# Performance work log

Measured on AMD Instinct MI355X. Metric: run time of the kernel, lower is better.

Reference implementation:

```python
import jax, jax.numpy as jnp
import numpy as np

D_MODEL = 768
N_HEAD = 12
D_FF = 3072
EPS = 1e-5


def _layer_norm(x, w, b):
    mu = jnp.mean(x, axis=-1, keepdims=True)
    var = jnp.mean(jnp.square(x - mu), axis=-1, keepdims=True)
    return (x - mu) * jax.lax.rsqrt(var + EPS) * w + b


def setup_inputs() -> dict:
    key = jax.random.key(0)
    ks = jax.random.split(key, 8)
    B, S, D = 2, 4096, D_MODEL
    s_in = 1.0 / np.sqrt(D)
    s_ff = 1.0 / np.sqrt(D_FF)
    return {
        "src": jax.random.normal(ks[0], (B, S, D), jnp.float32),
        "w_qkv": jax.random.uniform(ks[1], (3 * D, D), jnp.float32, -s_in, s_in),
        "b_qkv": jnp.zeros((3 * D,), jnp.float32),
        "w_out": jax.random.uniform(ks[2], (D, D), jnp.float32, -s_in, s_in),
        "b_out": jnp.zeros((D,), jnp.float32),
        "w1": jax.random.uniform(ks[3], (D_FF, D), jnp.float32, -s_in, s_in),
        "b1": jnp.zeros((D_FF,), jnp.float32),
        "w2": jax.random.uniform(ks[4], (D, D_FF), jnp.float32, -s_ff, s_ff),
        "b2": jnp.zeros((D,), jnp.float32),
        "ln1_w": jnp.ones((D,), jnp.float32),
        "ln1_b": jnp.zeros((D,), jnp.float32),
        "ln2_w": jnp.ones((D,), jnp.float32),
        "ln2_b": jnp.zeros((D,), jnp.float32),
    }


def reference(src, w_qkv, b_qkv, w_out, b_out, w1, b1, w2, b2,
              ln1_w, ln1_b, ln2_w, ln2_b):
    B, S, D = src.shape
    H, dh = N_HEAD, D // N_HEAD
    # fused QKV projection: [B,S,3D]
    qkv = jnp.einsum('bsd,ed->bse', src, w_qkv) + b_qkv
    q, k, v = jnp.split(qkv, 3, axis=-1)
    q = q.reshape(B, S, H, dh)
    k = k.reshape(B, S, H, dh)
    v = v.reshape(B, S, H, dh)
    scale = 1.0 / np.sqrt(dh)
    scores = jnp.einsum('bqhd,bkhd->bhqk', q, k) * scale  # [B,H,S,S]
    attn = jax.nn.softmax(scores, axis=-1)
    ctx = jnp.einsum('bhqk,bkhd->bqhd', attn, v).reshape(B, S, D)
    attn_out = jnp.einsum('bsd,ed->bse', ctx, w_out) + b_out
    # post-norm residual (norm_first=False), dropout inactive in eval
    x = _layer_norm(src + attn_out, ln1_w, ln1_b)
    h = jax.nn.relu(jnp.einsum('bsd,fd->bsf', x, w1) + b1)
    ffn = jnp.einsum('bsf,df->bsd', h, w2) + b2
    return _layer_norm(x + ffn, ln2_w, ln2_b)
```

## Files before the change

### kernel.cpp

```cpp
#include <hip/hip_runtime.h>
#include <hip/hip_bf16.h>

typedef __hip_bfloat16 bf16;
typedef __attribute__((ext_vector_type(8))) short s16x8;
typedef __attribute__((ext_vector_type(4))) float f32x4;

#define MFMA16x16x32(A, B, C) __builtin_amdgcn_mfma_f32_16x16x32_bf16((A), (B), (C), 0, 0, 0)

__device__ __forceinline__ void async_copy16(const bf16* g, bf16* l) {
  __builtin_amdgcn_global_load_lds(
      (const __attribute__((address_space(1))) void*)g,
      (__attribute__((address_space(3))) void*)l, 16, 0, 0);
}

__device__ __forceinline__ int SW(int row, int chunk) {
  return row * 64 + (((chunk) ^ (row & 7)) << 3);
}

__global__ __launch_bounds__(256)
void cast_f2b_kernel(const float* __restrict__ in, bf16* __restrict__ out, int n) {
  const int i = (blockIdx.x * 256 + threadIdx.x) * 4;
  if (i < n) {
    const float4 f = *(const float4*)(in + i);
    out[i + 0] = (bf16)f.x; out[i + 1] = (bf16)f.y;
    out[i + 2] = (bf16)f.z; out[i + 3] = (bf16)f.w;
  }
}

template <int RELU, int VT, int ACCUM, typename OutT>
__global__ __launch_bounds__(256)
void gemm_bt_kernel(const bf16* __restrict__ A, const bf16* __restrict__ B,
                    const float* __restrict__ bias, OutT* __restrict__ C,
                    int N, int K, int ldb) {
  __shared__ __align__(16) bf16 As[128 * 32];
  __shared__ __align__(16) bf16 Bs[128 * 32];

  const int t = threadIdx.x;
  const int lane = t & 63;
  const int wave = t >> 6;
  const int wm = (wave >> 1) << 6;
  const int wn = (wave & 1) << 6;
  const int col16 = lane & 15;
  const int quad = lane >> 4;
  const int bm = blockIdx.x;
  const int bn = blockIdx.y;

  const bf16* Ag = A + (size_t)(bm * 128 + (t >> 2)) * K + (t & 3) * 8;
  const bf16* Bg = B + (size_t)(bn * 128 + (t >> 2)) * ldb + (t & 3) * 8;
  bf16* Asd = As + t * 8;
  bf16* Bsd = Bs + t * 8;

  f32x4 acc[4][4] = {};

  for (int k0 = 0; k0 < K; k0 += 32) {
    __syncthreads();
    async_copy16(Ag + k0, Asd);
    async_copy16(Ag + (size_t)64 * K + k0, Asd + 2048);
    async_copy16(Bg + k0, Bsd);
    async_copy16(Bg + (size_t)64 * ldb + k0, Bsd + 2048);
    asm volatile("s_waitcnt vmcnt(0)" ::: "memory");
    __syncthreads();

    s16x8 af[4], bfr[4];
#pragma unroll
    for (int i = 0; i < 4; i++)
      af[i] = *(const s16x8*)(As + (wm + i * 16 + col16) * 32 + quad * 8);
#pragma unroll
    for (int j = 0; j < 4; j++)
      bfr[j] = *(const s16x8*)(Bs + (wn + j * 16 + col16) * 32 + quad * 8);
#pragma unroll
    for (int i = 0; i < 4; i++)
#pragma unroll
      for (int j = 0; j < 4; j++)
        acc[i][j] = MFMA16x16x32(af[i], bfr[j], acc[i][j]);
  }

  const int row0 = bm * 128 + wm + quad * 4;
  const int col0 = bn * 128 + wn + col16;
#pragma unroll
  for (int j = 0; j < 4; j++) {
    const int col = col0 + j * 16;
    const float bv = ACCUM ? 0.0f : bias[col];
#pragma unroll
    for (int i = 0; i < 4; i++) {
#pragma unroll
      for (int r = 0; r < 4; r++) {
        float v = acc[i][j][r] + bv;
        if (RELU) v = fmaxf(v, 0.0f);
        const int row = row0 + i * 16 + r;
        if (VT) {
          ((bf16*)C)[(size_t)((row >> 12) * 12 + (col >> 6)) * 262144 +
                     (col & 63) * 4096 + (row & 4095)] = (bf16)v;
        } else {
          const size_t idx = (size_t)row * N + col;
          if (ACCUM) v += ((const float*)C)[idx];
          C[idx] = (OutT)v;
        }
      }
    }
  }
}

__global__ __launch_bounds__(256)
void attn_kernel(const bf16* __restrict__ QK, const bf16* __restrict__ Vt,
                 bf16* __restrict__ Opart, float* __restrict__ lbuf) {
  __shared__ __align__(16) bf16 Ks[2][64 * 64];
  __shared__ __align__(16) bf16 Vs[2][64 * 64];
  __shared__ __align__(16) bf16 Ps[4][32 * 64];

  const int t = threadIdx.x, lane = t & 63, wave = t >> 6;
  const int col16 = lane & 15, quad = lane >> 4;
  const int b = blockIdx.z, h = blockIdx.y;
  const int ks = blockIdx.x >> 5;
  const int qblk = blockIdx.x & 31;
  const int qw0 = qblk * 128 + wave * 32;

  s16x8 bq[2][2];
#pragma unroll
  for (int qt = 0; qt < 2; qt++)
#pragma unroll
    for (int s = 0; s < 2; s++) {
      union { s16x8 v; bf16 hh[8]; } u;
      u.v = *(const s16x8*)(QK + (size_t)(b * 4096 + qw0 + qt * 16 + col16) * 1536 +
                            h * 64 + s * 32 + quad * 8);
#pragma unroll
      for (int e = 0; e < 8; e++) u.hh[e] = (bf16)((float)u.hh[e] * 0.18033688f);
      bq[qt][s] = u.v;
    }

  union { s16x8 v; short s_[8]; } uo1;
#pragma unroll
  for (int e = 0; e < 8; e++) uo1.s_[e] = (short)0x3F80;
  const s16x8 aones = uo1.v;

  const int srow = t >> 3;
  const int schx = (t & 7) ^ (srow & 7);
  const bf16* kgb = QK + (size_t)(b * 4096) * 1536 + 768 + h * 64;
  const bf16* vgb = Vt + (size_t)(b * 12 + h) * 262144;
  const bf16* ksrc0 = kgb + (size_t)srow * 1536 + schx * 8;
  const bf16* ksrc1 = kgb + (size_t)(32 + srow) * 1536 + schx * 8;
  const bf16* vsrc0 = vgb + (size_t)srow * 4096 + schx * 8;
  const bf16* vsrc1 = vgb + (size_t)(32 + srow) * 4096 + schx * 8;

  f32x4 o[4][2] = {};
  f32x4 lacc[2] = {};
  bf16* pw = &Ps[wave][0];

  const int kbeg = ks * 2048, kend = kbeg + 2048;

  async_copy16(ksrc0 + (size_t)kbeg * 1536, &Ks[0][0] + t * 8);
  async_copy16(ksrc1 + (size_t)kbeg * 1536, &Ks[0][0] + 2048 + t * 8);
  async_copy16(vsrc0 + kbeg, &Vs[0][0] + t * 8);
  async_copy16(vsrc1 + kbeg, &Vs[0][0] + 2048 + t * 8);

  int n = 0;
  for (int k0 = kbeg; k0 < kend; k0 += 64, n ^= 1) {
    __syncthreads();
    if (k0 + 64 < kend) {
      const int k1 = k0 + 64;
      async_copy16(ksrc0 + (size_t)k1 * 1536, &Ks[n ^ 1][0] + t * 8);
      async_copy16(ksrc1 + (size_t)k1 * 1536, &Ks[n ^ 1][0] + 2048 + t * 8);
      async_copy16(vsrc0 + k1, &Vs[n ^ 1][0] + t * 8);
      async_copy16(vsrc1 + k1, &Vs[n ^ 1][0] + 2048 + t * 8);
    }
    const bf16* ksn = &Ks[n][0];
    const bf16* vsn = &Vs[n][0];

    f32x4 st[4][2] = {};
#pragma unroll
    for (int s = 0; s < 2; s++) {
      s16x8 ak[4];
#pragma unroll
      for (int kt = 0; kt < 4; kt++)
        ak[kt] = *(const s16x8*)(ksn + SW(kt * 16 + col16, s * 4 + quad));
#pragma unroll
      for (int kt = 0; kt < 4; kt++)
#pragma unroll
        for (int qt = 0; qt < 2; qt++)
          st[kt][qt] = MFMA16x16x32(ak[kt], bq[qt][s], st[kt][qt]);
    }

#pragma unroll
    for (int qt = 0; qt < 2; qt++) {
#pragma unroll
      for (int kt = 0; kt < 4; kt++) {
        union { unsigned long long u; bf16 hh[4]; } pk;
#pragma unroll
        for (int r = 0; r < 4; r++)
          pk.hh[r] = (bf16)__builtin_amdgcn_exp2f(st[kt][qt][r]);
        *(unsigned long long*)(pw + (qt * 16 + col16) * 64 +
                               (((kt * 2 + (quad >> 1)) ^ (col16 & 7)) << 3) +
                               (quad & 1) * 4) = pk.u;
      }
    }
    asm volatile("s_waitcnt lgkmcnt(0)" ::: "memory");

#pragma unroll
    for (int s = 0; s < 2; s++) {
      s16x8 bp[2];
#pragma unroll
      for (int qt = 0; qt < 2; qt++)
        bp[qt] = *(const s16x8*)(pw + SW(qt * 16 + col16, s * 4 + quad));
#pragma unroll
      for (int qt = 0; qt < 2; qt++)
        lacc[qt] = MFMA16x16x32(aones, bp[qt], lacc[qt]);
#pragma unroll
      for (int dt = 0; dt < 4; dt++) {
        const s16x8 av = *(const s16x8*)(vsn + SW(dt * 16 + col16, s * 4 + quad));
#pragma unroll
        for (int qt = 0; qt < 2; qt++)
          o[dt][qt] = MFMA16x16x32(av, bp[qt], o[dt][qt]);
      }
    }
  }

  if (lane < 16) {
#pragma unroll
    for (int qt = 0; qt < 2; qt++)
      lbuf[(size_t)ks * 98304 + (size_t)(b * 4096 + qw0 + qt * 16 + lane) * 12 + h] =
          lacc[qt][0];
  }

#pragma unroll
  for (int qt = 0; qt < 2; qt++)
#pragma unroll
    for (int dt = 0; dt < 4; dt++)
#pragma unroll
      for (int r = 0; r < 4; r++)
        pw[(qt * 16 + col16) * 64 + (((dt * 2 + (quad >> 1)) ^ (col16 & 7)) << 3) +
           (quad & 1) * 4 + r] = (bf16)(o[dt][qt][r]);
  asm volatile("s_waitcnt lgkmcnt(0)" ::: "memory");
  const int qrow = lane >> 1, chalf = (lane & 1) * 4;
  bf16* dst = Opart + (size_t)ks * 6291456 +
              (size_t)(b * 4096 + qw0 + qrow) * 768 + h * 64 + chalf * 8;
#pragma unroll
  for (int i = 0; i < 4; i++)
    *(s16x8*)(dst + i * 8) = *(const s16x8*)(pw + SW(qrow, chalf + i));
}

__global__ __launch_bounds__(256)
void attn_combine_kernel(const bf16* __restrict__ Opart,
                         const float* __restrict__ lbuf,
                         bf16* __restrict__ ctx) {
  const int i = blockIdx.x * 256 + threadIdx.x;
  const int row = i / 96, c8 = i % 96;
  const int h = c8 >> 3;
  const float inv = 1.0f / (lbuf[(size_t)row * 12 + h] +
                            lbuf[98304 + (size_t)row * 12 + h]);
  union { s16x8 v; bf16 hh[8]; } ua, ub, uo;
  ua.v = *(const s16x8*)(Opart + (size_t)row * 768 + c8 * 8);
  ub.v = *(const s16x8*)(Opart + 6291456 + (size_t)row * 768 + c8 * 8);
#pragma unroll
  for (int j = 0; j < 8; j++)
    uo.hh[j] = (bf16)(((float)ua.hh[j] + (float)ub.hh[j]) * inv);
  *(s16x8*)(ctx + (size_t)row * 768 + c8 * 8) = uo.v;
}

__global__ __launch_bounds__(256)
void add_ln_b_kernel(const float* __restrict__ X, const float* __restrict__ Y,
                     const float* __restrict__ w, const float* __restrict__ b,
                     bf16* __restrict__ out) {
  const int row = blockIdx.x * 4 + (threadIdx.x >> 6);
  const int lane = threadIdx.x & 63;
  const float* x = X + (size_t)row * 768;
  const float* y = Y + (size_t)row * 768;
  float v[12];
  float s = 0.0f;
#pragma unroll
  for (int i = 0; i < 3; i++) {
    const int c = lane * 4 + i * 256;
    const float4 xf = *(const float4*)(x + c);
    const float4 yf = *(const float4*)(y + c);
    v[i * 4 + 0] = xf.x + yf.x; v[i * 4 + 1] = xf.y + yf.y;
    v[i * 4 + 2] = xf.z + yf.z; v[i * 4 + 3] = xf.w + yf.w;
    s += v[i * 4] + v[i * 4 + 1] + v[i * 4 + 2] + v[i * 4 + 3];
  }
#pragma unroll
  for (int off = 32; off > 0; off >>= 1) s += __shfl_xor(s, off, 64);
  const float mu = s * (1.0f / 768.0f);
  float var = 0.0f;
#pragma unroll
  for (int i = 0; i < 12; i++) { const float d = v[i] - mu; var += d * d; }
#pragma unroll
  for (int off = 32; off > 0; off >>= 1) var += __shfl_xor(var, off, 64);
  const float rs = rsqrtf(var * (1.0f / 768.0f) + 1e-5f);
#pragma unroll
  for (int i = 0; i < 12; i++) {
    const int c = lane * 4 + (i >> 2) * 256 + (i & 3);
    out[(size_t)row * 768 + c] = (bf16)((v[i] - mu) * rs * w[c] + b[c]);
  }
}

__global__ __launch_bounds__(256)
void add_ln_f_kernel(const bf16* __restrict__ X, const float* __restrict__ Y,
                     const float* __restrict__ w, const float* __restrict__ b,
                     float* __restrict__ out) {
  const int row = blockIdx.x * 4 + (threadIdx.x >> 6);
  const int lane = threadIdx.x & 63;
  const bf16* x = X + (size_t)row * 768;
  const float* y = Y + (size_t)row * 768;
  float v[12];
  float s = 0.0f;
#pragma unroll
  for (int i = 0; i < 3; i++) {
    const int c = lane * 4 + i * 256;
    const float4 yf = *(const float4*)(y + c);
    v[i * 4 + 0] = (float)x[c + 0] + yf.x; v[i * 4 + 1] = (float)x[c + 1] + yf.y;
    v[i * 4 + 2] = (float)x[c + 2] + yf.z; v[i * 4 + 3] = (float)x[c + 3] + yf.w;
    s += v[i * 4] + v[i * 4 + 1] + v[i * 4 + 2] + v[i * 4 + 3];
  }
#pragma unroll
  for (int off = 32; off > 0; off >>= 1) s += __shfl_xor(s, off, 64);
  const float mu = s * (1.0f / 768.0f);
  float var = 0.0f;
#pragma unroll
  for (int i = 0; i < 12; i++) { const float d = v[i] - mu; var += d * d; }
#pragma unroll
  for (int off = 32; off > 0; off >>= 1) var += __shfl_xor(var, off, 64);
  const float rs = rsqrtf(var * (1.0f / 768.0f) + 1e-5f);
#pragma unroll
  for (int i = 0; i < 12; i++) {
    const int c = lane * 4 + (i >> 2) * 256 + (i & 3);
    out[(size_t)row * 768 + c] = (v[i] - mu) * rs * w[c] + b[c];
  }
}

extern "C" void kernel_launch(void* const* d_in, const int* in_sizes, int n_in,
                              void* d_out, int out_size, void* d_ws, size_t ws_size,
                              hipStream_t stream) {
  (void)in_sizes; (void)n_in; (void)out_size; (void)ws_size;
  const float* src   = (const float*)d_in[0];
  const float* w_qkv = (const float*)d_in[1];
  const float* b_qkv = (const float*)d_in[2];
  const float* w_out = (const float*)d_in[3];
  const float* b_out = (const float*)d_in[4];
  const float* w1    = (const float*)d_in[5];
  const float* b1    = (const float*)d_in[6];
  const float* w2    = (const float*)d_in[7];
  const float* b2    = (const float*)d_in[8];
  const float* ln1w  = (const float*)d_in[9];
  const float* ln1b  = (const float*)d_in[10];
  const float* ln2w  = (const float*)d_in[11];
  const float* ln2b  = (const float*)d_in[12];
  float* out = (float*)d_out;

  char* ws = (char*)d_ws;
  bf16* wqkvb = (bf16*)ws;
  bf16* woutb = (bf16*)(ws + 3538944);
  bf16* w1b   = (bf16*)(ws + 4718592);
  bf16* w2b   = (bf16*)(ws + 9437184);
  bf16* srcb  = (bf16*)(ws + 14155776);
  bf16* QK    = (bf16*)(ws + 26738688);
  bf16* Vt    = (bf16*)(ws + 51904512);
  bf16* Opart = (bf16*)d_out;
  float* lbuf = (float*)ws;
  bf16* ctx   = (bf16*)(ws + 14155776);
  float* attn_out = (float*)(ws + 26738688);
  bf16* x1b   = (bf16*)(ws + 51904512);
  bf16* hbuf  = (bf16*)(ws + 14155776);
  float* ffn  = out;

  cast_f2b_kernel<<<1728, 256, 0, stream>>>(w_qkv, wqkvb, 2304 * 768);
  cast_f2b_kernel<<<576,  256, 0, stream>>>(w_out, woutb, 768 * 768);
  cast_f2b_kernel<<<2304, 256, 0, stream>>>(w1, w1b, 3072 * 768);
  cast_f2b_kernel<<<2304, 256, 0, stream>>>(w2, w2b, 768 * 3072);
  cast_f2b_kernel<<<6144, 256, 0, stream>>>(src, srcb, 8192 * 768);

  gemm_bt_kernel<0, 0, 0, bf16><<<dim3(64, 12), 256, 0, stream>>>(
      srcb, wqkvb, b_qkv, QK, 1536, 768, 768);
  gemm_bt_kernel<0, 1, 0, bf16><<<dim3(64, 6), 256, 0, stream>>>(
      srcb, wqkvb + (size_t)1536 * 768, b_qkv + 1536, Vt, 768, 768, 768);
  attn_kernel<<<dim3(64, 12, 2), 256, 0, stream>>>(QK, Vt, Opart, lbuf);
  attn_combine_kernel<<<3072, 256, 0, stream>>>(Opart, lbuf, ctx);
  gemm_bt_kernel<0, 0, 0, float><<<dim3(64, 6), 256, 0, stream>>>(
      ctx, woutb, b_out, attn_out, 768, 768, 768);
  add_ln_b_kernel<<<2048, 256, 0, stream>>>(src, attn_out, ln1w, ln1b, x1b);
  for (int c = 0; c < 2; c++) {
    gemm_bt_kernel<1, 0, 0, bf16><<<dim3(64, 12), 256, 0, stream>>>(
        x1b, w1b + (size_t)c * 1536 * 768, b1 + c * 1536, hbuf, 1536, 768, 768);
    if (c == 0)
      gemm_bt_kernel<0, 0, 0, float><<<dim3(64, 6), 256, 0, stream>>>(
          hbuf, w2b + c * 1536, b2, ffn, 768, 1536, 3072);
    else
      gemm_bt_kernel<0, 0, 1, float><<<dim3(64, 6), 256, 0, stream>>>(
          hbuf, w2b + c * 1536, b2, ffn, 768, 1536, 3072);
  }
  add_ln_f_kernel<<<2048, 256, 0, stream>>>(x1b, ffn, ln2w, ln2b, out);
}
```

Before: 494.3 us.

## Double-buffer GEMM LDS tiles and fuse QKV and V-transpose GEMM launches

The GEMM kernel now keeps two LDS buffers for the A and B tiles. It issues the async global-to-LDS copies for the next K step before computing on the current one, so load latency overlaps the MFMA work. The explicit vmcnt wait is dropped, so correctness depends on the barrier waiting for outstanding loads. Separately, the QK and V projections run as a single launch: an epilogue mode writes columns below 1536 row-major and the rest into the transposed V layout. This removes one launch and fills the grid better, at the cost of double the shared memory per block.

```diff
diff --git a/kernel.cpp b/kernel.cpp
--- a/kernel.cpp
+++ b/kernel.cpp
@@ -31,9 +31,9 @@
 __global__ __launch_bounds__(256)
 void gemm_bt_kernel(const bf16* __restrict__ A, const bf16* __restrict__ B,
                     const float* __restrict__ bias, OutT* __restrict__ C,
-                    int N, int K, int ldb) {
-  __shared__ __align__(16) bf16 As[128 * 32];
-  __shared__ __align__(16) bf16 Bs[128 * 32];
+                    int N, int K, int ldb, bf16* __restrict__ C2) {
+  __shared__ __align__(16) bf16 As[2][128 * 32];
+  __shared__ __align__(16) bf16 Bs[2][128 * 32];
 
   const int t = threadIdx.x;
   const int lane = t & 63;
@@ -47,27 +47,34 @@
 
   const bf16* Ag = A + (size_t)(bm * 128 + (t >> 2)) * K + (t & 3) * 8;
   const bf16* Bg = B + (size_t)(bn * 128 + (t >> 2)) * ldb + (t & 3) * 8;
-  bf16* Asd = As + t * 8;
-  bf16* Bsd = Bs + t * 8;
 
   f32x4 acc[4][4] = {};
 
-  for (int k0 = 0; k0 < K; k0 += 32) {
+  async_copy16(Ag, &As[0][0] + t * 8);
+  async_copy16(Ag + (size_t)64 * K, &As[0][0] + 2048 + t * 8);
+  async_copy16(Bg, &Bs[0][0] + t * 8);
+  async_copy16(Bg + (size_t)64 * ldb, &Bs[0][0] + 2048 + t * 8);
+
+  int n = 0;
+  for (int k0 = 0; k0 < K; k0 += 32, n ^= 1) {
     __syncthreads();
-    async_copy16(Ag + k0, Asd);
-    async_copy16(Ag + (size_t)64 * K + k0, Asd + 2048);
-    async_copy16(Bg + k0, Bsd);
-    async_copy16(Bg + (size_t)64 * ldb + k0, Bsd + 2048);
-    asm volatile("s_waitcnt vmcnt(0)" ::: "memory");
-    __syncthreads();
+    if (k0 + 32 < K) {
+      const int k1 = k0 + 32;
+      async_copy16(Ag + k1, &As[n ^ 1][0] + t * 8);
+      async_copy16(Ag + (size_t)64 * K + k1, &As[n ^ 1][0] + 2048 + t * 8);
+      async_copy16(Bg + k1, &Bs[n ^ 1][0] + t * 8);
+      async_copy16(Bg + (size_t)64 * ldb + k1, &Bs[n ^ 1][0] + 2048 + t * 8);
+    }
+    const bf16* asn = &As[n][0];
+    const bf16* bsn = &Bs[n][0];
 
     s16x8 af[4], bfr[4];
 #pragma unroll
     for (int i = 0; i < 4; i++)
-      af[i] = *(const s16x8*)(As + (wm + i * 16 + col16) * 32 + quad * 8);
+      af[i] = *(const s16x8*)(asn + (wm + i * 16 + col16) * 32 + quad * 8);
 #pragma unroll
     for (int j = 0; j < 4; j++)
-      bfr[j] = *(const s16x8*)(Bs + (wn + j * 16 + col16) * 32 + quad * 8);
+      bfr[j] = *(const s16x8*)(bsn + (wn + j * 16 + col16) * 32 + quad * 8);
 #pragma unroll
     for (int i = 0; i < 4; i++)
 #pragma unroll
@@ -88,9 +95,17 @@
         float v = acc[i][j][r] + bv;
         if (RELU) v = fmaxf(v, 0.0f);
         const int row = row0 + i * 16 + r;
-        if (VT) {
+        if (VT == 1) {
           ((bf16*)C)[(size_t)((row >> 12) * 12 + (col >> 6)) * 262144 +
                      (col & 63) * 4096 + (row & 4095)] = (bf16)v;
+        } else if (VT == 2) {
+          if (col < 1536) {
+            C[(size_t)row * N + col] = (OutT)v;
+          } else {
+            const int cc = col - 1536;
+            C2[(size_t)((row >> 12) * 12 + (cc >> 6)) * 262144 +
+               (cc & 63) * 4096 + (row & 4095)] = (bf16)v;
+          }
         } else {
           const size_t idx = (size_t)row * N + col;
           if (ACCUM) v += ((const float*)C)[idx];
@@ -366,24 +381,23 @@
   cast_f2b_kernel<<<2304, 256, 0, stream>>>(w2, w2b, 768 * 3072);
   cast_f2b_kernel<<<6144, 256, 0, stream>>>(src, srcb, 8192 * 768);
 
-  gemm_bt_kernel<0, 0, 0, bf16><<<dim3(64, 12), 256, 0, stream>>>(
-      srcb, wqkvb, b_qkv, QK, 1536, 768, 768);
-  gemm_bt_kernel<0, 1, 0, bf16><<<dim3(64, 6), 256, 0, stream>>>(
-      srcb, wqkvb + (size_t)1536 * 768, b_qkv + 1536, Vt, 768, 768, 768);
+  gemm_bt_kernel<0, 2, 0, bf16><<<dim3(64, 18), 256, 0, stream>>>(
+      srcb, wqkvb, b_qkv, QK, 1536, 768, 768, Vt);
   attn_kernel<<<dim3(64, 12, 2), 256, 0, stream>>>(QK, Vt, Opart, lbuf);
   attn_combine_kernel<<<3072, 256, 0, stream>>>(Opart, lbuf, ctx);
   gemm_bt_kernel<0, 0, 0, float><<<dim3(64, 6), 256, 0, stream>>>(
-      ctx, woutb, b_out, attn_out, 768, 768, 768);
+      ctx, woutb, b_out, attn_out, 768, 768, 768, nullptr);
   add_ln_b_kernel<<<2048, 256, 0, stream>>>(src, attn_out, ln1w, ln1b, x1b);
   for (int c = 0; c < 2; c++) {
     gemm_bt_kernel<1, 0, 0, bf16><<<dim3(64, 12), 256, 0, stream>>>(
-        x1b, w1b + (size_t)c * 1536 * 768, b1 + c * 1536, hbuf, 1536, 768, 768);
+        x1b, w1b + (size_t)c * 1536 * 768, b1 + c * 1536, hbuf, 1536, 768, 768,
+        nullptr);
     if (c == 0)
       gemm_bt_kernel<0, 0, 0, float><<<dim3(64, 6), 256, 0, stream>>>(
-          hbuf, w2b + c * 1536, b2, ffn, 768, 1536, 3072);
+          hbuf, w2b + c * 1536, b2, ffn, 768, 1536, 3072, nullptr);
     else
       gemm_bt_kernel<0, 0, 1, float><<<dim3(64, 6), 256, 0, stream>>>(
-          hbuf, w2b + c * 1536, b2, ffn, 768, 1536, 3072);
+          hbuf, w2b + c * 1536, b2, ffn, 768, 1536, 3072, nullptr);
   }
   add_ln_f_kernel<<<2048, 256, 0, stream>>>(x1b, ffn, ln2w, ln2b, out);
 }
```

New measurement: 498.1 us. Within noise of the previous version (+0.8%).
